# Kernel tuning notes

Hardware: AMD Instinct MI355X
Metric: run time of the kernel (lower is better)

Reference implementation:

```python
import jax, jax.numpy as jnp
import numpy as np

B, K, H, W = 8, 1024, 24, 24
C = H * W            # in_channels = 576
NH = 6               # hardcoded num_heads
HD = C // NH         # 96


def setup_inputs() -> dict:
    key = jax.random.key(0)
    ks = jax.random.split(key, 8)
    s = 1.0 / np.sqrt(C)
    return {
        "input1": jax.random.normal(ks[0], (B, K, H, W), jnp.float32),
        "input2": jax.random.normal(ks[1], (B, K, H, W), jnp.float32),
        "Wq": jax.random.uniform(ks[2], (C, C), jnp.float32, -s, s),
        "bq": jax.random.uniform(ks[3], (C,), jnp.float32, -s, s),
        "Wk": jax.random.uniform(ks[4], (C, C), jnp.float32, -s, s),
        "bk": jax.random.uniform(ks[5], (C,), jnp.float32, -s, s),
        "Wv": jax.random.uniform(ks[6], (C, C), jnp.float32, -s, s),
        "bv": jax.random.uniform(ks[7], (C,), jnp.float32, -s, s),
    }


def reference(input1, input2, Wq, bq, Wk, bk, Wv, bv):
    b, k, h, w = input1.shape
    c = h * w
    x1 = input1.reshape(b, k, c)
    x2 = input2.reshape(b, k, c)
    # torch nn.Linear: y = x @ W^T + b
    q = x1 @ Wq.T + bq                      # [b, k, c]
    kk = x2 @ Wk.T + bk
    v = x2 @ Wv.T + bv
    # torch .view scrambles: [b, k, c] -> [b, NH, c//NH, k] (row-major reshape)
    q = q.reshape(b, NH, c // NH, k)
    kk = kk.reshape(b, NH, c // NH, k)
    v = v.reshape(b, NH, c // NH, k)
    # scores = q^T k over head-dim; NOTE: no 1/sqrt(d) scaling in original
    scores = jnp.einsum('bhdq,bhdk->bhqk', q, kk)   # [b, NH, k, k]
    weights = jax.nn.softmax(scores, axis=-1)
    # context = value @ weights^T -> [b, NH, hd, k]
    ctx = jnp.einsum('bhdk,bhqk->bhdq', v, weights)
    return ctx.reshape(b, k, h, w)
```

## Files before the change

### kernel.cpp

```cpp
#include <hip/hip_runtime.h>
#include <cmath>

#define BATCH 8
#define KDIM  1024
#define CH    576
#define NHEAD 6
#define HDIM  96

typedef _Float16 f16;
typedef f16 f16x4 __attribute__((ext_vector_type(4)));
typedef f16 f16x8 __attribute__((ext_vector_type(8)));
typedef float f32x16 __attribute__((ext_vector_type(16)));
typedef unsigned int u32;

#define PSZ  (BATCH * KDIM * CH)
#define WSZ  (CH * CH)

__device__ inline f32x16 zero16() {
    f32x16 z;
#pragma unroll
    for (int r = 0; r < 16; ++r) z[r] = 0.f;
    return z;
}

__global__ __launch_bounds__(256) void convert_kernel(
    const float* __restrict__ x1, const float* __restrict__ x2,
    const float* __restrict__ Wq, const float* __restrict__ Wk,
    const float* __restrict__ Wv,
    f16* __restrict__ x1h, f16* __restrict__ x2h, f16* __restrict__ wh)
{
    const int y = blockIdx.y;
    int idx = blockIdx.x * 256 + threadIdx.x;
    const float* src;
    f16* dst;
    if (y == 0) {
        if (idx >= PSZ / 8) return;
        src = x1; dst = x1h;
    } else if (y == 1) {
        if (idx >= PSZ / 8) return;
        src = x2; dst = x2h;
    } else {
        if (idx >= 3 * WSZ / 8) return;
        int seg = idx / (WSZ / 8);
        src = (seg == 0) ? Wq : (seg == 1) ? Wk : Wv;
        dst = wh + seg * WSZ;
        idx -= seg * (WSZ / 8);
    }
    float4 u0 = ((const float4*)src)[2 * idx];
    float4 u1 = ((const float4*)src)[2 * idx + 1];
    f16x8 hv;
    hv[0] = (f16)u0.x; hv[1] = (f16)u0.y; hv[2] = (f16)u0.z; hv[3] = (f16)u0.w;
    hv[4] = (f16)u1.x; hv[5] = (f16)u1.y; hv[6] = (f16)u1.z; hv[7] = (f16)u1.w;
    ((f16x8*)dst)[idx] = hv;
}

__global__ __launch_bounds__(256, 4) void proj_kernel(
    const f16* __restrict__ x1h, const f16* __restrict__ x2h,
    const f16* __restrict__ wh,
    const float* __restrict__ bq, const float* __restrict__ bk,
    const float* __restrict__ bv,
    f16* __restrict__ qf, f16* __restrict__ kf, f16* __restrict__ vf)
{
    const int z = blockIdx.z;
    const f16* A      = (z == 0) ? x1h : x2h;
    const f16* W      = wh + z * WSZ;
    const float* bias = (z == 0) ? bq : (z == 1) ? bk : bv;
    f16* dst          = (z == 0) ? qf : (z == 1) ? kf : vf;

    __shared__ f16 As[64 * 72];
    __shared__ f16 Ws[192 * 72];

    const int tid = threadIdx.x;
    const int lane = tid & 63, w = tid >> 6;
    const int l31 = lane & 31, half = lane >> 5;
    const int mw = 32 * (w & 1), nh = 96 * (w >> 1);
    const int nBase = blockIdx.x * 192;
    const int mBase = blockIdx.y * 64;

    int arow[2], ach[2], wrow[6], wch[6];
#pragma unroll
    for (int r = 0; r < 2; ++r) {
        int idx = r * 256 + tid;
        arow[r] = idx >> 3; ach[r] = idx & 7;
    }
#pragma unroll
    for (int r = 0; r < 6; ++r) {
        int idx = r * 256 + tid;
        wrow[r] = idx >> 3; wch[r] = idx & 7;
    }

    f16x8 aP[2], wP[6];
#pragma unroll
    for (int r = 0; r < 2; ++r)
        aP[r] = *(const f16x8*)&A[(size_t)(mBase + arow[r]) * CH + ach[r] * 8];
#pragma unroll
    for (int r = 0; r < 6; ++r)
        wP[r] = *(const f16x8*)&W[(size_t)(nBase + wrow[r]) * CH + wch[r] * 8];

    f32x16 acc[3] = {zero16(), zero16(), zero16()};

    for (int k0 = 0; k0 < CH; k0 += 64) {
        __syncthreads();
#pragma unroll
        for (int r = 0; r < 2; ++r)
            *(f16x8*)&As[arow[r] * 72 + ach[r] * 8] = aP[r];
#pragma unroll
        for (int r = 0; r < 6; ++r)
            *(f16x8*)&Ws[wrow[r] * 72 + wch[r] * 8] = wP[r];
        __syncthreads();
        if (k0 + 64 < CH) {
#pragma unroll
            for (int r = 0; r < 2; ++r)
                aP[r] = *(const f16x8*)&A[(size_t)(mBase + arow[r]) * CH + k0 + 64 + ach[r] * 8];
#pragma unroll
            for (int r = 0; r < 6; ++r)
                wP[r] = *(const f16x8*)&W[(size_t)(nBase + wrow[r]) * CH + k0 + 64 + wch[r] * 8];
        }
#pragma unroll
        for (int ks = 0; ks < 4; ++ks) {
            f16x8 a = *(const f16x8*)&As[(mw + l31) * 72 + 16 * ks + 8 * half];
#pragma unroll
            for (int nt = 0; nt < 3; ++nt) {
                f16x8 bfr = *(const f16x8*)&Ws[(nh + 32 * nt + l31) * 72 + 16 * ks + 8 * half];
                acc[nt] = __builtin_amdgcn_mfma_f32_32x32x16_f16(a, bfr, acc[nt], 0, 0, 0);
            }
        }
    }

#pragma unroll
    for (int nt = 0; nt < 3; ++nt) {
        int n = nBase + nh + 32 * nt + l31;
        float bsv = bias[n];
#pragma unroll
        for (int r = 0; r < 16; ++r) {
            int m = mBase + mw + (r & 3) + 8 * (r >> 2) + 4 * half;
            dst[(size_t)m * CH + n] = (f16)(acc[nt][r] + bsv);
        }
    }
}

__global__ __launch_bounds__(256) void transpose_qk(
    const f16* __restrict__ qf, const f16* __restrict__ kf,
    f16* __restrict__ QT, f16* __restrict__ KT)
{
    const int tt = blockIdx.x;
    const int bh = blockIdx.y;
    const f16* src = blockIdx.z ? kf : qf;
    f16* dst = blockIdx.z ? KT : QT;

    __shared__ f16 Ts[96 * 72];

    const int tid = threadIdx.x;
    const int rowbase = (bh / NHEAD) * CH + (bh % NHEAD) * HDIM;

#pragma unroll
    for (int r = 0; r < 3; ++r) {
        int idx = r * 256 + tid;
        int d = idx >> 3, g = idx & 7;
        *(f16x8*)&Ts[d * 72 + g * 8] =
            *(const f16x8*)&src[(size_t)(rowbase + d) * KDIM + tt * 64 + g * 8];
    }
    __syncthreads();
#pragma unroll
    for (int r = 0; r < 3; ++r) {
        int idx = r * 256 + tid;
        int t = idx & 63, dg = idx >> 6;
        f16x8 v;
#pragma unroll
        for (int u = 0; u < 8; ++u) v[u] = Ts[(dg * 8 + u) * 72 + t];
        *(f16x8*)&dst[((size_t)bh * KDIM + tt * 64 + t) * HDIM + dg * 8] = v;
    }
}

__global__ __launch_bounds__(256, 3) void attn_kernel(
    const f16* __restrict__ qT, const f16* __restrict__ kT,
    const f16* __restrict__ vf, float* __restrict__ out)
{
    __shared__ __align__(16) char smem[27136];
    f16* Ks = (f16*)smem;
    f16* Vs = (f16*)(smem + 13312);
    f16* Qs = Ks;

    const int bh = blockIdx.x;
    const int qt = blockIdx.y;
    const int h  = bh % NHEAD;
    const int b  = bh / NHEAD;

    const int tid = threadIdx.x;
    const int lane = tid & 63, w = tid >> 6;
    const int ih = w & 1, jg = w >> 1;
    const int l31 = lane & 31, half = lane >> 5;
    const int iw = 32 * ih;

    const f16* Qbase = qT + ((size_t)bh * KDIM + qt * 64) * HDIM;
    const f16* Kbase = kT + (size_t)bh * KDIM * HDIM;
    const f16* Vbase = vf + ((size_t)b * CH + (size_t)h * HDIM) * KDIM;

    int kt[3], kg[3], vd[3], vg[3];
#pragma unroll
    for (int r = 0; r < 3; ++r) {
        int idx = r * 256 + tid;
        kt[r] = idx / 12; kg[r] = idx % 12;
        vd[r] = idx >> 3; vg[r] = idx & 7;
    }

#pragma unroll
    for (int r = 0; r < 3; ++r)
        *(f16x8*)&Qs[kt[r] * 104 + kg[r] * 8] =
            *(const f16x8*)&Qbase[kt[r] * 96 + kg[r] * 8];
    __syncthreads();
    f16x8 qfr[6];
#pragma unroll
    for (int ks = 0; ks < 6; ++ks) {
        qfr[ks] = *(const f16x8*)&Qs[(iw + l31) * 104 + 16 * ks + 8 * half];
#pragma unroll
        for (int u = 0; u < 8; ++u)
            qfr[ks][u] = (f16)((float)qfr[ks][u] * 1.44269504f);
    }

    f16x8 kreg[3], vreg[3];
#pragma unroll
    for (int r = 0; r < 3; ++r) {
        kreg[r] = *(const f16x8*)&Kbase[(size_t)kt[r] * HDIM + kg[r] * 8];
        vreg[r] = *(const f16x8*)&Vbase[(size_t)vd[r] * KDIM + vg[r] * 8];
    }

    float l_run = 0.f;
    f32x16 Oacc[3] = {zero16(), zero16(), zero16()};

    for (int jt = 0; jt < KDIM; jt += 64) {
        __syncthreads();
#pragma unroll
        for (int r = 0; r < 3; ++r) {
            *(f16x8*)&Ks[kt[r] * 104 + kg[r] * 8] = kreg[r];
            *(f16x8*)&Vs[vd[r] * 72 + vg[r] * 8]  = vreg[r];
        }
        __syncthreads();
        if (jt + 64 < KDIM) {
#pragma unroll
            for (int r = 0; r < 3; ++r) {
                kreg[r] = *(const f16x8*)&Kbase[(size_t)(jt + 64 + kt[r]) * HDIM + kg[r] * 8];
                vreg[r] = *(const f16x8*)&Vbase[(size_t)vd[r] * KDIM + jt + 64 + vg[r] * 8];
            }
        }

        f32x16 s0 = zero16();
#pragma unroll
        for (int ks = 0; ks < 6; ++ks) {
            f16x8 ak = *(const f16x8*)&Ks[(32 * jg + l31) * 104 + 16 * ks + 8 * half];
            s0 = __builtin_amdgcn_mfma_f32_32x32x16_f16(ak, qfr[ks], s0, 0, 0, 0);
        }

        f16x4 pq[4];
#pragma unroll
        for (int r = 0; r < 16; ++r) {
            float e = __builtin_amdgcn_exp2f(s0[r] - 26.0f);
            l_run += e;
            pq[r >> 2][r & 3] = (f16)e;
        }

#pragma unroll
        for (int kc = 0; kc < 2; ++kc) {
            union { f16x4 h; u32 u[2]; } snd, rcv, keep;
            keep.h = half ? pq[2 * kc + 1] : pq[2 * kc];
            snd.h  = half ? pq[2 * kc]     : pq[2 * kc + 1];
            rcv.u[0] = __shfl_xor((int)snd.u[0], 32);
            rcv.u[1] = __shfl_xor((int)snd.u[1], 32);
            f16x8 bp;
            if (half == 0) {
#pragma unroll
                for (int v = 0; v < 4; ++v) { bp[v] = keep.h[v]; bp[4 + v] = rcv.h[v]; }
            } else {
#pragma unroll
                for (int v = 0; v < 4; ++v) { bp[v] = rcv.h[v]; bp[4 + v] = keep.h[v]; }
            }
            int jo = 32 * jg + 16 * kc + 8 * half;
#pragma unroll
            for (int t = 0; t < 3; ++t) {
                f16x8 av = *(const f16x8*)&Vs[(32 * t + l31) * 72 + jo];
                Oacc[t] = __builtin_amdgcn_mfma_f32_32x32x16_f16(av, bp, Oacc[t], 0, 0, 0);
            }
        }
    }

    l_run += __shfl_xor(l_run, 32);

    __syncthreads();
    float* Oscr = (float*)smem;
    float* lScr = (float*)(smem + 25344);
    if (jg == 1) {
        if (half == 0) lScr[iw + l31] = l_run;
        float* od = Oscr + ih * 3168;
#pragma unroll
        for (int t = 0; t < 3; ++t)
#pragma unroll
            for (int r = 0; r < 16; ++r) {
                int d = 32 * t + (r & 3) + 8 * (r >> 2) + 4 * half;
                od[d * 33 + l31] = Oacc[t][r];
            }
    }
    __syncthreads();
    if (jg == 0) {
        float linv = 1.0f / (l_run + lScr[iw + l31]);
        const float* od = Oscr + ih * 3168;
        float* obase = out + ((size_t)b * CH + (size_t)h * HDIM) * KDIM
                           + qt * 64 + iw + l31;
#pragma unroll
        for (int t = 0; t < 3; ++t)
#pragma unroll
            for (int r = 0; r < 16; ++r) {
                int d = 32 * t + (r & 3) + 8 * (r >> 2) + 4 * half;
                obase[(size_t)d * KDIM] =
                    (Oacc[t][r] + od[d * 33 + l31]) * linv;
            }
    }
}

extern "C" void kernel_launch(void* const* d_in, const int* in_sizes, int n_in,
                              void* d_out, int out_size, void* d_ws, size_t ws_size,
                              hipStream_t stream)
{
    const float* x1 = (const float*)d_in[0];
    const float* x2 = (const float*)d_in[1];
    const float* Wq = (const float*)d_in[2];
    const float* bq = (const float*)d_in[3];
    const float* Wk = (const float*)d_in[4];
    const float* bk = (const float*)d_in[5];
    const float* Wv = (const float*)d_in[6];
    const float* bv = (const float*)d_in[7];
    float* out = (float*)d_out;

    const size_t P = PSZ;
    f16* x1h = (f16*)d_ws;
    f16* x2h = x1h + P;
    f16* qf  = x2h + P;
    f16* kf  = qf + P;
    f16* vf  = kf + P;
    f16* wh  = vf + P;
    f16* QT  = x1h;
    f16* KT  = x2h;

    dim3 cgrid((P / 8 + 255) / 256, 3);
    convert_kernel<<<cgrid, 256, 0, stream>>>(x1, x2, Wq, Wk, Wv, x1h, x2h, wh);

    dim3 pgrid(CH / 192, (BATCH * KDIM) / 64, 3);
    proj_kernel<<<pgrid, 256, 0, stream>>>(x1h, x2h, wh, bq, bk, bv, qf, kf, vf);

    dim3 tgrid(KDIM / 64, BATCH * NHEAD, 2);
    transpose_qk<<<tgrid, 256, 0, stream>>>(qf, kf, QT, KT);

    dim3 agrid(BATCH * NHEAD, KDIM / 64);
    attn_kernel<<<agrid, 256, 0, stream>>>(QT, KT, vf, out);
}
```

Measured before the change: 166.7 us.

## Double-buffer K/V tiles in shared memory to drop one barrier per iteration

The attention kernel now keeps two shared-memory buffers for the K and V tiles. During compute on the current tile it writes the prefetched next tile into the other buffer, so each iteration needs one __syncthreads instead of two. This doubles LDS use to about 53 KB per block, which may reduce how many blocks fit per CU under the launch bound of 3.

Measured after the change: 168.4 us. Within noise of the previous version (+1.0%).

```diff
diff --git a/kernel.cpp b/kernel.cpp
--- a/kernel.cpp
+++ b/kernel.cpp
@@ -176,10 +176,8 @@
     const f16* __restrict__ qT, const f16* __restrict__ kT,
     const f16* __restrict__ vf, float* __restrict__ out)
 {
-    __shared__ __align__(16) char smem[27136];
-    f16* Ks = (f16*)smem;
-    f16* Vs = (f16*)(smem + 13312);
-    f16* Qs = Ks;
+    __shared__ __align__(16) char smem[54272];
+    f16* Qs = (f16*)smem;
 
     const int bh = blockIdx.x;
     const int qt = blockIdx.y;
@@ -204,6 +202,13 @@
         vd[r] = idx >> 3; vg[r] = idx & 7;
     }
 
+    f16x8 kreg[3], vreg[3];
+#pragma unroll
+    for (int r = 0; r < 3; ++r) {
+        kreg[r] = *(const f16x8*)&Kbase[(size_t)kt[r] * HDIM + kg[r] * 8];
+        vreg[r] = *(const f16x8*)&Vbase[(size_t)vd[r] * KDIM + vg[r] * 8];
+    }
+
 #pragma unroll
     for (int r = 0; r < 3; ++r)
         *(f16x8*)&Qs[kt[r] * 104 + kg[r] * 8] =
@@ -217,37 +222,41 @@
         for (int u = 0; u < 8; ++u)
             qfr[ks][u] = (f16)((float)qfr[ks][u] * 1.44269504f);
     }
-
-    f16x8 kreg[3], vreg[3];
-#pragma unroll
-    for (int r = 0; r < 3; ++r) {
-        kreg[r] = *(const f16x8*)&Kbase[(size_t)kt[r] * HDIM + kg[r] * 8];
-        vreg[r] = *(const f16x8*)&Vbase[(size_t)vd[r] * KDIM + vg[r] * 8];
-    }
+    __syncthreads();
+
+    {
+        f16* Ks0 = (f16*)smem;
+        f16* Vs0 = (f16*)(smem + 26624);
+#pragma unroll
+        for (int r = 0; r < 3; ++r) {
+            *(f16x8*)&Ks0[kt[r] * 104 + kg[r] * 8] = kreg[r];
+            *(f16x8*)&Vs0[vd[r] * 72 + vg[r] * 8]  = vreg[r];
+        }
+    }
+    __syncthreads();
 
     float l_run = 0.f;
     f32x16 Oacc[3] = {zero16(), zero16(), zero16()};
 
-    for (int jt = 0; jt < KDIM; jt += 64) {
-        __syncthreads();
-#pragma unroll
-        for (int r = 0; r < 3; ++r) {
-            *(f16x8*)&Ks[kt[r] * 104 + kg[r] * 8] = kreg[r];
-            *(f16x8*)&Vs[vd[r] * 72 + vg[r] * 8]  = vreg[r];
-        }
-        __syncthreads();
-        if (jt + 64 < KDIM) {
+    for (int t = 0; t < 16; ++t) {
+        const int cur = t & 1;
+        f16* Ksc = (f16*)(smem + cur * 13312);
+        f16* Vsc = (f16*)(smem + 26624 + cur * 13824);
+
+        const bool more = (t + 1) < 16;
+        if (more) {
+            int jn = (t + 1) * 64;
 #pragma unroll
             for (int r = 0; r < 3; ++r) {
-                kreg[r] = *(const f16x8*)&Kbase[(size_t)(jt + 64 + kt[r]) * HDIM + kg[r] * 8];
-                vreg[r] = *(const f16x8*)&Vbase[(size_t)vd[r] * KDIM + jt + 64 + vg[r] * 8];
+                kreg[r] = *(const f16x8*)&Kbase[(size_t)(jn + kt[r]) * HDIM + kg[r] * 8];
+                vreg[r] = *(const f16x8*)&Vbase[(size_t)vd[r] * KDIM + jn + vg[r] * 8];
             }
         }
 
         f32x16 s0 = zero16();
 #pragma unroll
         for (int ks = 0; ks < 6; ++ks) {
-            f16x8 ak = *(const f16x8*)&Ks[(32 * jg + l31) * 104 + 16 * ks + 8 * half];
+            f16x8 ak = *(const f16x8*)&Ksc[(32 * jg + l31) * 104 + 16 * ks + 8 * half];
             s0 = __builtin_amdgcn_mfma_f32_32x32x16_f16(ak, qfr[ks], s0, 0, 0, 0);
         }
 
@@ -276,27 +285,37 @@
             }
             int jo = 32 * jg + 16 * kc + 8 * half;
 #pragma unroll
-            for (int t = 0; t < 3; ++t) {
-                f16x8 av = *(const f16x8*)&Vs[(32 * t + l31) * 72 + jo];
-                Oacc[t] = __builtin_amdgcn_mfma_f32_32x32x16_f16(av, bp, Oacc[t], 0, 0, 0);
-            }
-        }
+            for (int tt = 0; tt < 3; ++tt) {
+                f16x8 av = *(const f16x8*)&Vsc[(32 * tt + l31) * 72 + jo];
+                Oacc[tt] = __builtin_amdgcn_mfma_f32_32x32x16_f16(av, bp, Oacc[tt], 0, 0, 0);
+            }
+        }
+
+        if (more) {
+            f16* Ksn = (f16*)(smem + (1 - cur) * 13312);
+            f16* Vsn = (f16*)(smem + 26624 + (1 - cur) * 13824);
+#pragma unroll
+            for (int r = 0; r < 3; ++r) {
+                *(f16x8*)&Ksn[kt[r] * 104 + kg[r] * 8] = kreg[r];
+                *(f16x8*)&Vsn[vd[r] * 72 + vg[r] * 8]  = vreg[r];
+            }
+        }
+        __syncthreads();
     }
 
     l_run += __shfl_xor(l_run, 32);
 
-    __syncthreads();
     float* Oscr = (float*)smem;
     float* lScr = (float*)(smem + 25344);
     if (jg == 1) {
         if (half == 0) lScr[iw + l31] = l_run;
         float* od = Oscr + ih * 3168;
 #pragma unroll
-        for (int t = 0; t < 3; ++t)
+        for (int tt = 0; tt < 3; ++tt)
 #pragma unroll
             for (int r = 0; r < 16; ++r) {
-                int d = 32 * t + (r & 3) + 8 * (r >> 2) + 4 * half;
-                od[d * 33 + l31] = Oacc[t][r];
+                int d = 32 * tt + (r & 3) + 8 * (r >> 2) + 4 * half;
+                od[d * 33 + l31] = Oacc[tt][r];
             }
     }
     __syncthreads();
@@ -306,12 +325,12 @@
         float* obase = out + ((size_t)b * CH + (size_t)h * HDIM) * KDIM
                            + qt * 64 + iw + l31;
 #pragma unroll
-        for (int t = 0; t < 3; ++t)
+        for (int tt = 0; tt < 3; ++tt)
 #pragma unroll
             for (int r = 0; r < 16; ++r) {
-                int d = 32 * t + (r & 3) + 8 * (r >> 2) + 4 * half;
+                int d = 32 * tt + (r & 3) + 8 * (r >> 2) + 4 * half;
                 obase[(size_t)d * KDIM] =
-                    (Oacc[t][r] + od[d * 33 + l31]) * linv;
+                    (Oacc[tt][r] + od[d * 33 + l31]) * linv;
             }
     }
 }
```
